# Performance work log

Measured on AMD Instinct MI355X. Metric: run time of the kernel, lower is better.

Reference implementation:

```python
import jax, jax.numpy as jnp
import numpy as np

N = 100000      # nodes
DEG = 16        # fixed degree
E = N * DEG     # edges
C_IN = 128
C_OUT = 128


def setup_inputs() -> dict:
    key = jax.random.key(0)
    k1, k2, k3, k4, k5 = jax.random.split(key, 5)
    x = jax.random.normal(k1, (N, C_IN), dtype=jnp.float32)
    # glorot-ish init for the dense weight
    scale = jnp.sqrt(6.0 / (C_IN + C_OUT)).astype(jnp.float32)
    weight = jax.random.uniform(k2, (C_IN, C_OUT), dtype=jnp.float32, minval=-1.0, maxval=1.0) * scale
    bias = jax.random.normal(k3, (C_OUT,), dtype=jnp.float32) * 0.02
    # fixed-degree CSR: every node has DEG in-edges; CSC analogously
    rowptr = (jnp.arange(N + 1, dtype=jnp.int32) * DEG)
    colind = jax.random.randint(k4, (E,), 0, N, dtype=jnp.int32)
    colptr = (jnp.arange(N + 1, dtype=jnp.int32) * DEG)
    rowind = jax.random.randint(k5, (E,), 0, N, dtype=jnp.int32)
    return {"x": x, "weight": weight, "bias": bias,
            "rowptr": rowptr, "colind": colind,
            "colptr": colptr, "rowind": rowind}


def _deg_inv_sqrt(indptr, dtype):
    deg = (indptr[1:] - indptr[:-1]).astype(dtype)
    return (1.0 / jnp.sqrt(deg))[:, None]  # [N, 1]


def reference(x, weight, bias, rowptr, colind, colptr, rowind):
    # dense transform: [N, C_in] @ [C_in, C_out]
    h = x @ weight
    in_norm = _deg_inv_sqrt(rowptr, h.dtype)    # 1/sqrt(in-degree)
    out_norm = _deg_inv_sqrt(colptr, h.dtype)   # 1/sqrt(out-degree)
    h = h * out_norm
    # CSR SpMM (unweighted): out[i] = sum_{e in [rowptr[i], rowptr[i+1])} h[colind[e]]
    n_nodes = rowptr.shape[0] - 1
    n_edges = colind.shape[0]
    row = jnp.searchsorted(rowptr, jnp.arange(n_edges, dtype=rowptr.dtype), side="right") - 1
    aggr = jax.ops.segment_sum(h[colind], row, num_segments=n_nodes)
    aggr = aggr * in_norm + bias
    return aggr
```

## Files before the change

### kernel.cpp

```cpp
#include <hip/hip_runtime.h>
#include <hip/hip_bf16.h>

#define N_NODES 100000
#define DEG 16
#define C 128
#define NTILES 6250
#define GEMM_BLOCKS 256
#define GEMM_WAVES 8

typedef __attribute__((ext_vector_type(8))) short short8;
typedef __attribute__((ext_vector_type(4))) float f32x4;

__device__ inline unsigned short f2bf(float f) {
    unsigned int u = __builtin_bit_cast(unsigned int, f);
    u += 0x7fffu + ((u >> 16) & 1u);
    return (unsigned short)(u >> 16);
}

__global__ __launch_bounds__(256, 8)
void gcn_prep_kernel(const float* __restrict__ x, const int* __restrict__ colptr,
                     unsigned char* __restrict__ x8, float* __restrict__ scale)
{
    int tid = threadIdx.x;
    int wave = tid >> 6;
    int lane = tid & 63;
    int row = (blockIdx.x * 4 + wave) * 4 + (lane >> 4);
    int cg = lane & 15;

    const float* xr = x + (long)row * C + cg * 8;
    f32x4 a = *reinterpret_cast<const f32x4*>(xr);
    f32x4 b = *reinterpret_cast<const f32x4*>(xr + 4);

    float m = fmaxf(fmaxf(fmaxf(fabsf(a[0]), fabsf(a[1])), fmaxf(fabsf(a[2]), fabsf(a[3]))),
                    fmaxf(fmaxf(fabsf(b[0]), fabsf(b[1])), fmaxf(fabsf(b[2]), fabsf(b[3]))));
    m = fmaxf(m, __shfl_xor(m, 1));
    m = fmaxf(m, __shfl_xor(m, 2));
    m = fmaxf(m, __shfl_xor(m, 4));
    m = fmaxf(m, __shfl_xor(m, 8));
    m = fmaxf(m, 1e-30f);

    float inv = 127.0f / m;
    unsigned int lo = 0, hi = 0;
    lo |= ((unsigned int)((int)rintf(a[0] * inv) + 128));
    lo |= ((unsigned int)((int)rintf(a[1] * inv) + 128)) << 8;
    lo |= ((unsigned int)((int)rintf(a[2] * inv) + 128)) << 16;
    lo |= ((unsigned int)((int)rintf(a[3] * inv) + 128)) << 24;
    hi |= ((unsigned int)((int)rintf(b[0] * inv) + 128));
    hi |= ((unsigned int)((int)rintf(b[1] * inv) + 128)) << 8;
    hi |= ((unsigned int)((int)rintf(b[2] * inv) + 128)) << 16;
    hi |= ((unsigned int)((int)rintf(b[3] * inv) + 128)) << 24;

    uint2 pk; pk.x = lo; pk.y = hi;
    *reinterpret_cast<uint2*>(x8 + (long)row * C + cg * 8) = pk;

    if (cg == 0) {
        int od = colptr[row + 1] - colptr[row];
        scale[row] = m * (1.0f / 127.0f) * rsqrtf((float)od);
    }
}

__global__ __launch_bounds__(256, 8)
void gcn_aggr_kernel(const unsigned char* __restrict__ x8,
                     const float* __restrict__ scale,
                     const int* __restrict__ rowptr,
                     const int* __restrict__ colind,
                     unsigned short* __restrict__ agg)
{
    int tid = threadIdx.x;
    int wave = tid >> 6;
    int lane = tid & 63;
    int g  = lane >> 4;
    int cl = lane & 15;

    int node = (blockIdx.x * 4 + wave) * 4 + g;

    int base = rowptr[node];
    int deg  = rowptr[node + 1] - base;
    float innorm = rsqrtf((float)deg);

    int myidx = colind[base + cl];
    float myscale = scale[myidx];

    int gb = lane & 48;
    uint2 v[16];
#pragma unroll
    for (int e = 0; e < 16; ++e) {
        int j = __shfl(myidx, gb + e);
        v[e] = *reinterpret_cast<const uint2*>(x8 + (long)j * C + cl * 8);
    }

    float acc[8];
#pragma unroll
    for (int i = 0; i < 8; ++i) acc[i] = 0.f;
    float ssum = 0.f;

#pragma unroll
    for (int e = 0; e < 16; ++e) {
        float s = __shfl(myscale, gb + e);
        ssum += s;
        unsigned int a = v[e].x, b = v[e].y;
        acc[0] += s * (float)(a & 0xff);
        acc[1] += s * (float)((a >> 8) & 0xff);
        acc[2] += s * (float)((a >> 16) & 0xff);
        acc[3] += s * (float)(a >> 24);
        acc[4] += s * (float)(b & 0xff);
        acc[5] += s * (float)((b >> 8) & 0xff);
        acc[6] += s * (float)((b >> 16) & 0xff);
        acc[7] += s * (float)(b >> 24);
    }

    float fix = 128.0f * ssum;
    uint4 o;
    o.x = (unsigned int)f2bf((acc[0] - fix) * innorm) |
          ((unsigned int)f2bf((acc[1] - fix) * innorm) << 16);
    o.y = (unsigned int)f2bf((acc[2] - fix) * innorm) |
          ((unsigned int)f2bf((acc[3] - fix) * innorm) << 16);
    o.z = (unsigned int)f2bf((acc[4] - fix) * innorm) |
          ((unsigned int)f2bf((acc[5] - fix) * innorm) << 16);
    o.w = (unsigned int)f2bf((acc[6] - fix) * innorm) |
          ((unsigned int)f2bf((acc[7] - fix) * innorm) << 16);
    *reinterpret_cast<uint4*>(agg + (long)node * C + cl * 8) = o;
}

__global__ __launch_bounds__(512, 2)
void gcn_gemm_kernel(const unsigned short* __restrict__ agg, const float* __restrict__ w,
                     const float* __restrict__ bias, float* __restrict__ out)
{
    __shared__ unsigned short wfrag[32 * 64 * 8];

    int tid = threadIdx.x;
    for (int i = tid; i < C * C; i += 512) {
        int k = i >> 7, n = i & 127;
        int nt = n >> 4, lr = n & 15;
        int kc = k >> 5, quad = (k >> 3) & 3, j = k & 7;
        wfrag[((((nt << 2) + kc) << 6) + (quad << 4) + lr) * 8 + j] = f2bf(w[i]);
    }
    __syncthreads();

    int wave = tid >> 6;
    int lane = tid & 63;
    int lrow = lane & 15;
    int quad = lane >> 4;

    short8 bf[8][4];
#pragma unroll
    for (int nt = 0; nt < 8; ++nt)
#pragma unroll
        for (int kc = 0; kc < 4; ++kc)
            bf[nt][kc] = *reinterpret_cast<const short8*>(
                &wfrag[((((nt << 2) + kc) << 6) + lane) * 8]);

    float bv[8];
#pragma unroll
    for (int nt = 0; nt < 8; ++nt) bv[nt] = bias[nt * 16 + lrow];

    int tile = blockIdx.x * GEMM_WAVES + wave;
    if (tile >= NTILES) return;
    const int tstride = GEMM_BLOCKS * GEMM_WAVES;

    short8 af[4];
    {
        const unsigned short* ar = agg + (long)(tile * 16 + lrow) * C + quad * 8;
#pragma unroll
        for (int kc = 0; kc < 4; ++kc)
            af[kc] = *reinterpret_cast<const short8*>(ar + kc * 32);
    }

    while (true) {
        int m0 = tile * 16;
        short8 cur[4];
#pragma unroll
        for (int kc = 0; kc < 4; ++kc) cur[kc] = af[kc];

        int next = tile + tstride;
        bool more = next < NTILES;
        if (more) {
            const unsigned short* ar = agg + (long)(next * 16 + lrow) * C + quad * 8;
#pragma unroll
            for (int kc = 0; kc < 4; ++kc)
                af[kc] = *reinterpret_cast<const short8*>(ar + kc * 32);
        }

#pragma unroll
        for (int nt = 0; nt < 8; ++nt) {
            f32x4 acc = {0.f, 0.f, 0.f, 0.f};
#pragma unroll
            for (int kc = 0; kc < 4; ++kc)
                acc = __builtin_amdgcn_mfma_f32_16x16x32_bf16(cur[kc], bf[nt][kc], acc, 0, 0, 0);
            float* op = out + (long)(m0 + quad * 4) * C + nt * 16 + lrow;
#pragma unroll
            for (int r = 0; r < 4; ++r)
                op[r * C] = acc[r] + bv[nt];
        }
        if (!more) break;
        tile = next;
    }
}

extern "C" void kernel_launch(void* const* d_in, const int* in_sizes, int n_in,
                              void* d_out, int out_size, void* d_ws, size_t ws_size,
                              hipStream_t stream) {
    const float* x      = (const float*)d_in[0];
    const float* w      = (const float*)d_in[1];
    const float* bias   = (const float*)d_in[2];
    const int*   rowptr = (const int*)d_in[3];
    const int*   colind = (const int*)d_in[4];
    const int*   colptr = (const int*)d_in[5];
    float* out = (float*)d_out;

    unsigned char* x8    = (unsigned char*)d_out;
    float*         scale = (float*)((char*)d_out + (size_t)N_NODES * C);
    unsigned short* agg  = (unsigned short*)d_ws;

    gcn_prep_kernel<<<6250, 256, 0, stream>>>(x, colptr, x8, scale);
    gcn_aggr_kernel<<<6250, 256, 0, stream>>>(x8, scale, rowptr, colind, agg);
    gcn_gemm_kernel<<<GEMM_BLOCKS, 512, 0, stream>>>(agg, w, bias, out);
}
```

Before: 157.5 us.

## Fuse gather-aggregation and bf16 MFMA GEMM into one persistent double-buffered kernel

Merges the int8 neighbor aggregation and the dense GEMM into one persistent kernel. Each block aggregates a 16-node tile into a swizzled LDS buffer, then multiplies it by weight fragments held in registers, so the bf16 intermediate no longer round-trips through global memory. The next tile's gathers are issued before the current tile's MFMAs to overlap gather latency with compute. The quantized x8/scale buffers move from the output buffer to workspace. In exchange, each block rebuilds bf16 weight fragments from strided global reads, and there is one __syncthreads per tile.

After: 155.8 us. About the same (-1.1%).

```diff
diff --git a/kernel.cpp b/kernel.cpp
--- a/kernel.cpp
+++ b/kernel.cpp
@@ -5,8 +5,7 @@
 #define DEG 16
 #define C 128
 #define NTILES 6250
-#define GEMM_BLOCKS 256
-#define GEMM_WAVES 8
+#define FBLOCKS 1024
 
 typedef __attribute__((ext_vector_type(8))) short short8;
 typedef __attribute__((ext_vector_type(4))) float f32x4;
@@ -59,44 +58,13 @@
     }
 }
 
-__global__ __launch_bounds__(256, 8)
-void gcn_aggr_kernel(const unsigned char* __restrict__ x8,
-                     const float* __restrict__ scale,
-                     const int* __restrict__ rowptr,
-                     const int* __restrict__ colind,
-                     unsigned short* __restrict__ agg)
+__device__ __forceinline__ uint4 dq_pack(const uint2* v, float mysc, int gb, float innorm)
 {
-    int tid = threadIdx.x;
-    int wave = tid >> 6;
-    int lane = tid & 63;
-    int g  = lane >> 4;
-    int cl = lane & 15;
-
-    int node = (blockIdx.x * 4 + wave) * 4 + g;
-
-    int base = rowptr[node];
-    int deg  = rowptr[node + 1] - base;
-    float innorm = rsqrtf((float)deg);
-
-    int myidx = colind[base + cl];
-    float myscale = scale[myidx];
-
-    int gb = lane & 48;
-    uint2 v[16];
+    float acc[8] = {0.f, 0.f, 0.f, 0.f, 0.f, 0.f, 0.f, 0.f};
+    float ssum = 0.f;
 #pragma unroll
     for (int e = 0; e < 16; ++e) {
-        int j = __shfl(myidx, gb + e);
-        v[e] = *reinterpret_cast<const uint2*>(x8 + (long)j * C + cl * 8);
-    }
-
-    float acc[8];
-#pragma unroll
-    for (int i = 0; i < 8; ++i) acc[i] = 0.f;
-    float ssum = 0.f;
-
-#pragma unroll
-    for (int e = 0; e < 16; ++e) {
-        float s = __shfl(myscale, gb + e);
+        float s = __shfl(mysc, gb + e);
         ssum += s;
         unsigned int a = v[e].x, b = v[e].y;
         acc[0] += s * (float)(a & 0xff);
@@ -108,7 +76,6 @@
         acc[6] += s * (float)((b >> 16) & 0xff);
         acc[7] += s * (float)(b >> 24);
     }
-
     float fix = 128.0f * ssum;
     uint4 o;
     o.x = (unsigned int)f2bf((acc[0] - fix) * innorm) |
@@ -119,81 +86,109 @@
           ((unsigned int)f2bf((acc[5] - fix) * innorm) << 16);
     o.w = (unsigned int)f2bf((acc[6] - fix) * innorm) |
           ((unsigned int)f2bf((acc[7] - fix) * innorm) << 16);
-    *reinterpret_cast<uint4*>(agg + (long)node * C + cl * 8) = o;
-}
-
-__global__ __launch_bounds__(512, 2)
-void gcn_gemm_kernel(const unsigned short* __restrict__ agg, const float* __restrict__ w,
-                     const float* __restrict__ bias, float* __restrict__ out)
+    return o;
+}
+
+__global__ __launch_bounds__(256, 4)
+void gcn_fused_kernel(const unsigned char* __restrict__ x8,
+                      const float* __restrict__ scale,
+                      const int* __restrict__ rowptr,
+                      const int* __restrict__ colind,
+                      const float* __restrict__ wmat,
+                      const float* __restrict__ bias,
+                      float* __restrict__ out)
 {
-    __shared__ unsigned short wfrag[32 * 64 * 8];
-
-    int tid = threadIdx.x;
-    for (int i = tid; i < C * C; i += 512) {
-        int k = i >> 7, n = i & 127;
-        int nt = n >> 4, lr = n & 15;
-        int kc = k >> 5, quad = (k >> 3) & 3, j = k & 7;
-        wfrag[((((nt << 2) + kc) << 6) + (quad << 4) + lr) * 8 + j] = f2bf(w[i]);
+    __shared__ uint4 atile[2][16 * 16];
+
+    int tid  = threadIdx.x;
+    int wv   = tid >> 6;
+    int lane = tid & 63;
+    int g    = lane >> 4;
+    int cl   = lane & 15;
+    int gb   = lane & 48;
+
+    short8 bw[2][4];
+    float  bv[2];
+#pragma unroll
+    for (int n = 0; n < 2; ++n) {
+        int nt = wv * 2 + n;
+#pragma unroll
+        for (int kc = 0; kc < 4; ++kc) {
+            short8 b;
+#pragma unroll
+            for (int j = 0; j < 8; ++j)
+                b[j] = (short)f2bf(wmat[(kc * 32 + g * 8 + j) * C + nt * 16 + cl]);
+            bw[n][kc] = b;
+        }
+        bv[n] = bias[nt * 16 + cl];
+    }
+
+    int t = blockIdx.x;
+
+    {
+        int node = t * 16 + wv * 4 + g;
+        int base = rowptr[node];
+        float innorm = rsqrtf((float)(rowptr[node + 1] - base));
+        int myidx = colind[base + cl];
+        float mysc = scale[myidx];
+        uint2 v[16];
+#pragma unroll
+        for (int e = 0; e < 16; ++e) {
+            int j = __shfl(myidx, gb + e);
+            v[e] = *reinterpret_cast<const uint2*>(x8 + (j << 7) + (cl << 3));
+        }
+        int r = wv * 4 + g;
+        atile[0][r * 16 + (cl ^ (r & 7))] = dq_pack(v, mysc, gb, innorm);
     }
     __syncthreads();
 
-    int wave = tid >> 6;
-    int lane = tid & 63;
-    int lrow = lane & 15;
-    int quad = lane >> 4;
-
-    short8 bf[8][4];
-#pragma unroll
-    for (int nt = 0; nt < 8; ++nt)
+    int p = 0;
+    while (true) {
+        int nxt = t + FBLOCKS;
+        bool more = nxt < NTILES;
+
+        int nidx = 0; float nsc = 0.f, ninn = 0.f;
+        uint2 nv[16];
+        if (more) {
+            int nn = nxt * 16 + wv * 4 + g;
+            int nb = rowptr[nn];
+            ninn = rsqrtf((float)(rowptr[nn + 1] - nb));
+            nidx = colind[nb + cl];
+            nsc = scale[nidx];
+#pragma unroll
+            for (int e = 0; e < 16; ++e) {
+                int j = __shfl(nidx, gb + e);
+                nv[e] = *reinterpret_cast<const uint2*>(x8 + (j << 7) + (cl << 3));
+            }
+        }
+
+        short8 af[4];
 #pragma unroll
         for (int kc = 0; kc < 4; ++kc)
-            bf[nt][kc] = *reinterpret_cast<const short8*>(
-                &wfrag[((((nt << 2) + kc) << 6) + lane) * 8]);
-
-    float bv[8];
-#pragma unroll
-    for (int nt = 0; nt < 8; ++nt) bv[nt] = bias[nt * 16 + lrow];
-
-    int tile = blockIdx.x * GEMM_WAVES + wave;
-    if (tile >= NTILES) return;
-    const int tstride = GEMM_BLOCKS * GEMM_WAVES;
-
-    short8 af[4];
-    {
-        const unsigned short* ar = agg + (long)(tile * 16 + lrow) * C + quad * 8;
-#pragma unroll
-        for (int kc = 0; kc < 4; ++kc)
-            af[kc] = *reinterpret_cast<const short8*>(ar + kc * 32);
-    }
-
-    while (true) {
-        int m0 = tile * 16;
-        short8 cur[4];
-#pragma unroll
-        for (int kc = 0; kc < 4; ++kc) cur[kc] = af[kc];
-
-        int next = tile + tstride;
-        bool more = next < NTILES;
-        if (more) {
-            const unsigned short* ar = agg + (long)(next * 16 + lrow) * C + quad * 8;
+            af[kc] = __builtin_bit_cast(short8,
+                atile[p][cl * 16 + ((kc * 4 + g) ^ (cl & 7))]);
+
+#pragma unroll
+        for (int n = 0; n < 2; ++n) {
+            f32x4 acc = {0.f, 0.f, 0.f, 0.f};
 #pragma unroll
             for (int kc = 0; kc < 4; ++kc)
-                af[kc] = *reinterpret_cast<const short8*>(ar + kc * 32);
-        }
-
-#pragma unroll
-        for (int nt = 0; nt < 8; ++nt) {
-            f32x4 acc = {0.f, 0.f, 0.f, 0.f};
-#pragma unroll
-            for (int kc = 0; kc < 4; ++kc)
-                acc = __builtin_amdgcn_mfma_f32_16x16x32_bf16(cur[kc], bf[nt][kc], acc, 0, 0, 0);
-            float* op = out + (long)(m0 + quad * 4) * C + nt * 16 + lrow;
-#pragma unroll
-            for (int r = 0; r < 4; ++r)
-                op[r * C] = acc[r] + bv[nt];
-        }
+                acc = __builtin_amdgcn_mfma_f32_16x16x32_bf16(af[kc], bw[n][kc], acc, 0, 0, 0);
+            float* op = out + (long)(t * 16 + g * 4) * C + (wv * 2 + n) * 16 + cl;
+#pragma unroll
+            for (int r2 = 0; r2 < 4; ++r2)
+                op[r2 * C] = acc[r2] + bv[n];
+        }
+
         if (!more) break;
-        tile = next;
+
+        {
+            int r = wv * 4 + g;
+            atile[p ^ 1][r * 16 + (cl ^ (r & 7))] = dq_pack(nv, nsc, gb, ninn);
+        }
+        __syncthreads();
+        t = nxt;
+        p ^= 1;
     }
 }
 
@@ -208,11 +203,10 @@
     const int*   colptr = (const int*)d_in[5];
     float* out = (float*)d_out;
 
-    unsigned char* x8    = (unsigned char*)d_out;
-    float*         scale = (float*)((char*)d_out + (size_t)N_NODES * C);
-    unsigned short* agg  = (unsigned short*)d_ws;
+    unsigned char* x8    = (unsigned char*)d_ws;
+    float*         scale = (float*)((char*)d_ws + (size_t)N_NODES * C);
 
     gcn_prep_kernel<<<6250, 256, 0, stream>>>(x, colptr, x8, scale);
-    gcn_aggr_kernel<<<6250, 256, 0, stream>>>(x8, scale, rowptr, colind, agg);
-    gcn_gemm_kernel<<<GEMM_BLOCKS, 512, 0, stream>>>(agg, w, bias, out);
-}
+    gcn_fused_kernel<<<FBLOCKS, 256, 0, stream>>>(x8, scale, rowptr, colind,
+                                                  w, bias, out);
+}
```
